# Optimization experiments

Measured on AMD Instinct MI355X. Metric: run time of the kernel, lower is better.

## Reference

```python
import jax, jax.numpy as jnp
import numpy as np

B, S, D, H = 2, 2048, 1024, 16
HD = D // H  # head_dim = 64
THETA = 10000.0


def setup_inputs() -> dict:
    key = jax.random.key(0)
    ks = jax.random.split(key, 7)
    sd = 1.0 / np.sqrt(D)
    return {
        "hidden_states": jax.random.normal(ks[0], (B, S, D), jnp.float32),
        "attention_mask": jnp.ones((B, S), jnp.int32),
        "Wq": jax.random.normal(ks[1], (D, D), jnp.float32) * sd,
        "Wk": jax.random.normal(ks[2], (D, D), jnp.float32) * sd,
        "Wv": jax.random.normal(ks[3], (D, D), jnp.float32) * sd,
        "Wo": jax.random.normal(ks[4], (D, D), jnp.float32) * sd,
        "bo": jnp.zeros((D,), jnp.float32),
        "rel_bias": jax.random.normal(ks[5], (H, S, S), jnp.float32) * 0.02,
    }


def _rope_tables(seq_len):
    inv_freq = 1.0 / (THETA ** (jnp.arange(0, HD, 2, dtype=jnp.float32) / HD))  # [HD/2]
    freqs = jnp.arange(seq_len, dtype=jnp.float32)[:, None] * inv_freq[None, :]  # [S, HD/2]
    # add a heads axis for broadcasting against [B, S, H, HD/2]
    return jnp.cos(freqs)[:, None, :], jnp.sin(freqs)[:, None, :]


def _apply_rope(x, cos, sin):
    # x: [B, S, H, HD]; interleaved even/odd rotation
    x1, x2 = x[..., 0::2], x[..., 1::2]
    r1 = x1 * cos - x2 * sin
    r2 = x1 * sin + x2 * cos
    return jnp.stack([r1, r2], axis=-1).reshape(x.shape)


def reference(hidden_states, attention_mask, Wq, Wk, Wv, Wo, bo, rel_bias):
    b, s, d = hidden_states.shape
    q = (hidden_states @ Wq.T).reshape(b, s, H, HD)
    k = (hidden_states @ Wk.T).reshape(b, s, H, HD)
    v = (hidden_states @ Wv.T).reshape(b, s, H, HD)

    cos, sin = _rope_tables(s)
    q = _apply_rope(q, cos, sin)
    k = _apply_rope(k, cos, sin)

    scale = HD ** -0.5
    scores = jnp.einsum('bqhd,bkhd->bhqk', q, k) * scale + rel_bias[None]
    scores = jnp.where(attention_mask[:, None, None, :] == 0, -jnp.inf, scores)
    attn = jax.nn.softmax(scores, axis=-1)  # dropout is identity in eval
    out = jnp.einsum('bhqk,bkhd->bqhd', attn, v).reshape(b, s, d)
    return out @ Wo.T + bo
```

## Files before the change

kernel.cpp:

```cpp
#include <hip/hip_runtime.h>

typedef unsigned short u16;
typedef short bf16x8 __attribute__((ext_vector_type(8)));
typedef float f32x4 __attribute__((ext_vector_type(4)));
typedef unsigned short u16x4 __attribute__((ext_vector_type(4)));

typedef const __attribute__((address_space(1))) unsigned int* gas_ptr;
typedef __attribute__((address_space(3))) unsigned int* las_ptr;

__device__ __forceinline__ void gl_lds16(const void* g, void* l) {
  __builtin_amdgcn_global_load_lds((gas_ptr)g, (las_ptr)l, 16, 0, 0);
}

__device__ __forceinline__ u16 f2bf(float f) {
  union { float f; unsigned u; } v; v.f = f;
  unsigned r = v.u + 0x7FFFu + ((v.u >> 16) & 1u);
  return (u16)(r >> 16);
}

__global__ void k_rope_tables(float* __restrict__ ctab, float* __restrict__ stab) {
  int t = blockIdx.x * 256 + threadIdx.x;
  int s = t >> 5, tt = t & 31;
  double f = exp(-((double)(2 * tt) / 64.0) * log(10000.0));
  double a = (double)s * f;
  ctab[t] = (float)cos(a);
  stab[t] = (float)sin(a);
}

__device__ __forceinline__ void store_bf4(u16* p, float4 v) {
  u16x4 o; o[0] = f2bf(v.x); o[1] = f2bf(v.y); o[2] = f2bf(v.z); o[3] = f2bf(v.w);
  *(u16x4*)p = o;
}

__global__ void k_convert(const float* __restrict__ hs, const float* __restrict__ Wq,
                          const float* __restrict__ Wk, const float* __restrict__ Wv,
                          const float* __restrict__ Wo,
                          u16* __restrict__ Xb, u16* __restrict__ Wqkv, u16* __restrict__ Wob) {
  int e = (blockIdx.x * 256 + threadIdx.x) * 4;
  const int R1 = 4096 * 1024, R2 = R1 + 3072 * 1024;
  if (e < R1) {
    store_bf4(Xb + e, *(const float4*)&hs[e]);
  } else if (e < R2) {
    int w = e - R1; int row = w >> 10, col = w & 1023;
    const float* src = row < 1024 ? &Wq[(size_t)row * 1024]
                     : (row < 2048 ? &Wk[(size_t)(row - 1024) * 1024]
                                   : &Wv[(size_t)(row - 2048) * 1024]);
    store_bf4(Wqkv + w, *(const float4*)&src[col]);
  } else {
    int w = e - R2;
    store_bf4(Wob + w, *(const float4*)&Wo[w]);
  }
}

__global__ __launch_bounds__(256, 3)
void k_gemm_bt(const u16* __restrict__ A, const u16* __restrict__ B,
               const float* __restrict__ bias, float* __restrict__ C,
               int K, int ldc) {
  __shared__ u16 ldsA[128 * 64];
  __shared__ u16 ldsB[128 * 64];
  const int tid = threadIdx.x;
  const int bn = blockIdx.x, bm = blockIdx.y;
  const int lane = tid & 63, wave = tid >> 6;
  const int wm = wave >> 1, wn = wave & 1;
  const int l16 = lane & 15, quad = lane >> 4;

  const int srow = lane >> 3;
  const int scol = ((lane & 7) ^ srow) * 8;
  const u16* agb = A + (size_t)(bm * 128 + wave * 8 + srow) * K + scol;
  const u16* bgb = B + (size_t)(bn * 128 + wave * 8 + srow) * K + scol;

  const f32x4 vzero = {0.f, 0.f, 0.f, 0.f};
  f32x4 acc[4][4];
#pragma unroll
  for (int i = 0; i < 4; ++i)
#pragma unroll
    for (int j = 0; j < 4; ++j) acc[i][j] = vzero;

  const int xq = l16 & 7;
  const int NKT = K >> 6;
  for (int kt = 0; kt < NKT; ++kt) {
    __syncthreads();
#pragma unroll
    for (int p = 0; p < 4; ++p) {
      gl_lds16(agb + (size_t)p * 32 * K + kt * 64, &ldsA[(p * 4 + wave) * 512]);
      gl_lds16(bgb + (size_t)p * 32 * K + kt * 64, &ldsB[(p * 4 + wave) * 512]);
    }
    __syncthreads();
#pragma unroll
    for (int ks = 0; ks < 2; ++ks) {
      bf16x8 af[4], bfr[4];
#pragma unroll
      for (int mi = 0; mi < 4; ++mi)
        af[mi] = *(const bf16x8*)&ldsA[(wm * 64 + mi * 16 + l16) * 64 + ((ks * 4 + quad) ^ xq) * 8];
#pragma unroll
      for (int ni = 0; ni < 4; ++ni)
        bfr[ni] = *(const bf16x8*)&ldsB[(wn * 64 + ni * 16 + l16) * 64 + ((ks * 4 + quad) ^ xq) * 8];
#pragma unroll
      for (int mi = 0; mi < 4; ++mi)
#pragma unroll
        for (int ni = 0; ni < 4; ++ni)
          acc[mi][ni] = __builtin_amdgcn_mfma_f32_16x16x32_bf16(af[mi], bfr[ni], acc[mi][ni], 0, 0, 0);
    }
  }

  const int row0 = bm * 128 + wm * 64, col0 = bn * 128 + wn * 64;
#pragma unroll
  for (int mi = 0; mi < 4; ++mi)
#pragma unroll
    for (int ni = 0; ni < 4; ++ni) {
      int col = col0 + ni * 16 + l16;
      float badd = bias ? bias[col] : 0.f;
#pragma unroll
      for (int rr = 0; rr < 4; ++rr) {
        int row = row0 + mi * 16 + quad * 4 + rr;
        C[(size_t)row * ldc + col] = acc[mi][ni][rr] + badd;
      }
    }
}

__global__ void k_rope_apply(const float* __restrict__ QKV, const float* __restrict__ ctab,
                             const float* __restrict__ stab,
                             u16* __restrict__ Qb, u16* __restrict__ Kb) {
  int t = blockIdx.x * 256 + threadIdx.x;
  int i = t >> 9;
  int c = t & 511; int h = c >> 5, tt = c & 31;
  int s = i & 2047, b = i >> 11;
  const float* base = QKV + (size_t)i * 3072;
  float cs = ctab[s * 32 + tt], sn = stab[s * 32 + tt];
  float2 q = *(const float2*)&base[h * 64 + 2 * tt];
  float2 k = *(const float2*)&base[1024 + h * 64 + 2 * tt];
  size_t ob = ((size_t)(b * 16 + h) * 2048 + s) * 64 + 2 * tt;
  union { u16 h2[2]; unsigned u; } oq, ok;
  oq.h2[0] = f2bf((q.x * cs - q.y * sn) * 0.125f);
  oq.h2[1] = f2bf((q.x * sn + q.y * cs) * 0.125f);
  ok.h2[0] = f2bf(k.x * cs - k.y * sn);
  ok.h2[1] = f2bf(k.x * sn + k.y * cs);
  *(unsigned*)&Qb[ob] = oq.u;
  *(unsigned*)&Kb[ob] = ok.u;
}

__global__ void k_vtrans(const float* __restrict__ QKV, u16* __restrict__ Vtb) {
  __shared__ u16 T[64 * 72];
  int st = blockIdx.x & 31, bh = blockIdx.x >> 5;
  int tid = threadIdx.x;
  int b = bh >> 4, h = bh & 15;
  {
    int rr = tid >> 2;
    int dg = (tid & 3) * 16;
    const float* src = QKV + (size_t)(b * 2048 + st * 64 + rr) * 3072 + 2048 + h * 64 + dg;
#pragma unroll
    for (int j = 0; j < 4; ++j) {
      float4 v = *(const float4*)&src[j * 4];
      T[(dg + j * 4 + 0) * 72 + rr] = f2bf(v.x);
      T[(dg + j * 4 + 1) * 72 + rr] = f2bf(v.y);
      T[(dg + j * 4 + 2) * 72 + rr] = f2bf(v.z);
      T[(dg + j * 4 + 3) * 72 + rr] = f2bf(v.w);
    }
  }
  __syncthreads();
  int d = tid >> 2, cg = (tid & 3) * 2;
  u16* vo = Vtb + ((size_t)bh * 64 + d) * 2048 + st * 64;
  *(float4*)&vo[cg * 8]       = *(const float4*)&T[d * 72 + cg * 8];
  *(float4*)&vo[(cg + 1) * 8] = *(const float4*)&T[d * 72 + (cg + 1) * 8];
}

__global__ __launch_bounds__(256, 4)
void k_attn(const u16* __restrict__ Qb, const u16* __restrict__ Kb, const u16* __restrict__ Vtb,
            const float* __restrict__ rel_bias, const int* __restrict__ mask,
            u16* __restrict__ Ob) {
  __shared__ u16 Ks[2][64 * 64];
  __shared__ u16 Vs[2][64 * 64];
  __shared__ u16 Ps[64 * 64];

  const int tid = threadIdx.x;
  const int gid = blockIdx.x;
  const int b = gid & 1, h = (gid >> 1) & 15, qt = gid >> 5;
  const int bh = b * 16 + h;
  const int lane = tid & 63, w = tid >> 6;
  const int l16 = lane & 15, quad = lane >> 4;
  const int xq = l16 & 7;

  bf16x8 qreg[2];
  {
    const u16* qg = Qb + ((size_t)bh * 2048 + qt * 64 + w * 16 + l16) * 64 + quad * 8;
    qreg[0] = *(const bf16x8*)&qg[0];
    qreg[1] = *(const bf16x8*)&qg[32];
  }

  const int srow = lane >> 3;
  const int scol = ((lane & 7) ^ srow) * 8;
  const u16* kgb = Kb + ((size_t)bh * 2048 + w * 8 + srow) * 64 + scol;
  const u16* vgb = Vtb + ((size_t)bh * 64 + w * 8 + srow) * 2048 + scol;

  const float* bp[4];
#pragma unroll
  for (int rr = 0; rr < 4; ++rr)
    bp[rr] = rel_bias + ((size_t)h * 2048 + qt * 64 + w * 16 + quad * 4 + rr) * 2048 + l16;
  const int* mbase = mask + b * 2048 + l16;

  const f32x4 vzero = {0.f, 0.f, 0.f, 0.f};
  f32x4 accO[4];
  float ls[4] = {0.f, 0.f, 0.f, 0.f};
#pragma unroll
  for (int ni = 0; ni < 4; ++ni) accO[ni] = vzero;

  float brc[4][4], brn[4][4];
  int mkc[4], mkn[4];
#pragma unroll
  for (int ni = 0; ni < 4; ++ni) {
    mkc[ni] = mbase[ni * 16];
#pragma unroll
    for (int rr = 0; rr < 4; ++rr) brc[ni][rr] = bp[rr][ni * 16];
  }
  gl_lds16(kgb,               &Ks[0][(0 * 4 + w) * 512]);
  gl_lds16(kgb + 2048,        &Ks[0][(1 * 4 + w) * 512]);
  gl_lds16(vgb,               &Vs[0][(0 * 4 + w) * 512]);
  gl_lds16(vgb + 32 * 2048,   &Vs[0][(1 * 4 + w) * 512]);

  for (int t = 0; t < 32; ++t) {
    const int cur = t & 1, nxt = cur ^ 1;
    const int kt0 = t * 64;
    __syncthreads();

    if (t + 1 < 32) {
      gl_lds16(kgb + (kt0 + 64) * 64,        &Ks[nxt][(0 * 4 + w) * 512]);
      gl_lds16(kgb + (kt0 + 64) * 64 + 2048, &Ks[nxt][(1 * 4 + w) * 512]);
      gl_lds16(vgb + kt0 + 64,               &Vs[nxt][(0 * 4 + w) * 512]);
      gl_lds16(vgb + kt0 + 64 + 32 * 2048,   &Vs[nxt][(1 * 4 + w) * 512]);
#pragma unroll
      for (int ni = 0; ni < 4; ++ni) {
        mkn[ni] = mbase[kt0 + 64 + ni * 16];
#pragma unroll
        for (int rr = 0; rr < 4; ++rr) brn[ni][rr] = bp[rr][kt0 + 64 + ni * 16];
      }
    }

    f32x4 sa[4];
#pragma unroll
    for (int ni = 0; ni < 4; ++ni) sa[ni] = vzero;
#pragma unroll
    for (int ks = 0; ks < 2; ++ks) {
#pragma unroll
      for (int ni = 0; ni < 4; ++ni) {
        bf16x8 kf = *(const bf16x8*)&Ks[cur][(ni * 16 + l16) * 64 + ((ks * 4 + quad) ^ xq) * 8];
        sa[ni] = __builtin_amdgcn_mfma_f32_16x16x32_bf16(qreg[ks], kf, sa[ni], 0, 0, 0);
      }
    }

#pragma unroll
    for (int ni = 0; ni < 4; ++ni) {
#pragma unroll
      for (int rr = 0; rr < 4; ++rr) {
        float p = mkc[ni] ? __expf(sa[ni][rr] + brc[ni][rr] - 24.f) : 0.f;
        int prow = w * 16 + quad * 4 + rr;
        Ps[prow * 64 + (((ni * 2 + (l16 >> 3)) ^ (prow & 7)) << 3) + (l16 & 7)] = f2bf(p);
        ls[rr] += p;
      }
    }

#pragma unroll
    for (int ks = 0; ks < 2; ++ks) {
      bf16x8 pf = *(const bf16x8*)&Ps[(w * 16 + l16) * 64 + ((ks * 4 + quad) ^ xq) * 8];
#pragma unroll
      for (int ni = 0; ni < 4; ++ni) {
        bf16x8 vf = *(const bf16x8*)&Vs[cur][(ni * 16 + l16) * 64 + ((ks * 4 + quad) ^ xq) * 8];
        accO[ni] = __builtin_amdgcn_mfma_f32_16x16x32_bf16(pf, vf, accO[ni], 0, 0, 0);
      }
    }

#pragma unroll
    for (int ni = 0; ni < 4; ++ni) {
      mkc[ni] = mkn[ni];
#pragma unroll
      for (int rr = 0; rr < 4; ++rr) brc[ni][rr] = brn[ni][rr];
    }
  }

#pragma unroll
  for (int rr = 0; rr < 4; ++rr) {
#pragma unroll
    for (int d = 1; d < 16; d <<= 1) ls[rr] += __shfl_xor(ls[rr], d, 16);
  }
#pragma unroll
  for (int rr = 0; rr < 4; ++rr) {
    float inv = 1.f / ls[rr];
    int row = qt * 64 + w * 16 + quad * 4 + rr;
#pragma unroll
    for (int ni = 0; ni < 4; ++ni)
      Ob[(((size_t)b * 2048 + row) * 16 + h) * 64 + ni * 16 + l16] = f2bf(accO[ni][rr] * inv);
  }
}

extern "C" void kernel_launch(void* const* d_in, const int* in_sizes, int n_in,
                              void* d_out, int out_size, void* d_ws, size_t ws_size,
                              hipStream_t stream) {
  (void)in_sizes; (void)n_in; (void)out_size; (void)ws_size;
  const float* hs  = (const float*)d_in[0];
  const int*   msk = (const int*)d_in[1];
  const float* Wq  = (const float*)d_in[2];
  const float* Wk  = (const float*)d_in[3];
  const float* Wv  = (const float*)d_in[4];
  const float* Wo  = (const float*)d_in[5];
  const float* bo  = (const float*)d_in[6];
  const float* rb  = (const float*)d_in[7];
  float* out = (float*)d_out;

  char* ws = (char*)d_ws;
  size_t off = 0;
  auto alloc = [&](size_t n) { char* p = ws + off; off += (n + 255) & ~(size_t)255; return p; };
  float* QKV  = (float*)alloc(4096UL * 3072 * 4);
  u16*   Xb   = (u16*)  alloc(4096UL * 1024 * 2);
  u16*   Wqkv = (u16*)  alloc(3072UL * 1024 * 2);
  u16*   Wob  = (u16*)  alloc(1024UL * 1024 * 2);
  u16*   Qb   = (u16*)  alloc(4096UL * 1024 * 2);
  u16*   Kb   = (u16*)  alloc(4096UL * 1024 * 2);
  u16*   Vtb  = (u16*)  alloc(4096UL * 1024 * 2);
  float* ctab = (float*)alloc(2048UL * 32 * 4);
  float* stab = (float*)alloc(2048UL * 32 * 4);
  u16*   Ob   = Xb;

  k_rope_tables<<<256, 256, 0, stream>>>(ctab, stab);
  k_convert<<<8192, 256, 0, stream>>>(hs, Wq, Wk, Wv, Wo, Xb, Wqkv, Wob);
  k_gemm_bt<<<dim3(24, 32), 256, 0, stream>>>(Xb, Wqkv, nullptr, QKV, 1024, 3072);
  k_rope_apply<<<8192, 256, 0, stream>>>(QKV, ctab, stab, Qb, Kb);
  k_vtrans<<<1024, 256, 0, stream>>>(QKV, Vtb);
  k_attn<<<1024, 256, 0, stream>>>(Qb, Kb, Vtb, rb, msk, Ob);
  k_gemm_bt<<<dim3(8, 32), 256, 0, stream>>>(Ob, Wob, bo, out, 1024, 1024);
}
```

Before: 523.6 us.

## Fuse RoPE and V transpose into QKV GEMM epilogue, fold tables into convert

Merges the RoPE table computation into the convert kernel. RoPE, the Q scale and the V transpose become part of the QKV GEMM epilogue, which writes bf16 Q/K/Vt directly. This removes the fp32 QKV intermediate and two extra kernel launches. The attention softmax switches to exp2 with the bias pre-scaled and the mask folded into the bias registers, and the block order now iterates heads fastest. The output projection uses a new 128x64-tile GEMM to double the block count. Risks include scattered strided stores for Vt in the epilogue and redundant table loads per element.

```diff
diff --git a/kernel.cpp b/kernel.cpp
--- a/kernel.cpp
+++ b/kernel.cpp
@@ -18,44 +18,47 @@
   return (u16)(r >> 16);
 }
 
-__global__ void k_rope_tables(float* __restrict__ ctab, float* __restrict__ stab) {
-  int t = blockIdx.x * 256 + threadIdx.x;
-  int s = t >> 5, tt = t & 31;
-  double f = exp(-((double)(2 * tt) / 64.0) * log(10000.0));
-  double a = (double)s * f;
-  ctab[t] = (float)cos(a);
-  stab[t] = (float)sin(a);
-}
-
-__device__ __forceinline__ void store_bf4(u16* p, float4 v) {
-  u16x4 o; o[0] = f2bf(v.x); o[1] = f2bf(v.y); o[2] = f2bf(v.z); o[3] = f2bf(v.w);
-  *(u16x4*)p = o;
+__device__ __forceinline__ float fexp2(float x) {
+  float r; asm("v_exp_f32 %0, %1" : "=v"(r) : "v"(x)); return r;
 }
 
 __global__ void k_convert(const float* __restrict__ hs, const float* __restrict__ Wq,
                           const float* __restrict__ Wk, const float* __restrict__ Wv,
                           const float* __restrict__ Wo,
-                          u16* __restrict__ Xb, u16* __restrict__ Wqkv, u16* __restrict__ Wob) {
+                          u16* __restrict__ Xb, u16* __restrict__ Wqkv, u16* __restrict__ Wob,
+                          float* __restrict__ ctab, float* __restrict__ stab) {
+  if (blockIdx.x >= 8192) {
+    int t = (blockIdx.x - 8192) * 256 + threadIdx.x;
+    int s = t >> 5, tt = t & 31;
+    double f = exp(-((double)(2 * tt) / 64.0) * log(10000.0));
+    double a = (double)s * f;
+    ctab[t] = (float)cos(a);
+    stab[t] = (float)sin(a);
+    return;
+  }
   int e = (blockIdx.x * 256 + threadIdx.x) * 4;
   const int R1 = 4096 * 1024, R2 = R1 + 3072 * 1024;
+  float4 v; u16* dst;
   if (e < R1) {
-    store_bf4(Xb + e, *(const float4*)&hs[e]);
+    v = *(const float4*)&hs[e]; dst = Xb + e;
   } else if (e < R2) {
     int w = e - R1; int row = w >> 10, col = w & 1023;
     const float* src = row < 1024 ? &Wq[(size_t)row * 1024]
                      : (row < 2048 ? &Wk[(size_t)(row - 1024) * 1024]
                                    : &Wv[(size_t)(row - 2048) * 1024]);
-    store_bf4(Wqkv + w, *(const float4*)&src[col]);
+    v = *(const float4*)&src[col]; dst = Wqkv + w;
   } else {
-    int w = e - R2;
-    store_bf4(Wob + w, *(const float4*)&Wo[w]);
-  }
+    int w = e - R2; v = *(const float4*)&Wo[w]; dst = Wob + w;
+  }
+  u16x4 o; o[0] = f2bf(v.x); o[1] = f2bf(v.y); o[2] = f2bf(v.z); o[3] = f2bf(v.w);
+  *(u16x4*)dst = o;
 }
 
 __global__ __launch_bounds__(256, 3)
-void k_gemm_bt(const u16* __restrict__ A, const u16* __restrict__ B,
-               const float* __restrict__ bias, float* __restrict__ C,
-               int K, int ldc) {
+void k_gemm_qkv(const u16* __restrict__ A, const u16* __restrict__ B,
+                const float* __restrict__ ctab, const float* __restrict__ stab,
+                u16* __restrict__ Qb, u16* __restrict__ Kb, u16* __restrict__ Vtb,
+                int K) {
   __shared__ u16 ldsA[128 * 64];
   __shared__ u16 ldsB[128 * 64];
   const int tid = threadIdx.x;
@@ -104,64 +107,52 @@
   }
 
   const int row0 = bm * 128 + wm * 64, col0 = bn * 128 + wn * 64;
-#pragma unroll
-  for (int mi = 0; mi < 4; ++mi)
-#pragma unroll
-    for (int ni = 0; ni < 4; ++ni) {
-      int col = col0 + ni * 16 + l16;
-      float badd = bias ? bias[col] : 0.f;
-#pragma unroll
-      for (int rr = 0; rr < 4; ++rr) {
-        int row = row0 + mi * 16 + quad * 4 + rr;
-        C[(size_t)row * ldc + col] = acc[mi][ni][rr] + badd;
-      }
-    }
-}
-
-__global__ void k_rope_apply(const float* __restrict__ QKV, const float* __restrict__ ctab,
-                             const float* __restrict__ stab,
-                             u16* __restrict__ Qb, u16* __restrict__ Kb) {
-  int t = blockIdx.x * 256 + threadIdx.x;
-  int i = t >> 9;
-  int c = t & 511; int h = c >> 5, tt = c & 31;
-  int s = i & 2047, b = i >> 11;
-  const float* base = QKV + (size_t)i * 3072;
-  float cs = ctab[s * 32 + tt], sn = stab[s * 32 + tt];
-  float2 q = *(const float2*)&base[h * 64 + 2 * tt];
-  float2 k = *(const float2*)&base[1024 + h * 64 + 2 * tt];
-  size_t ob = ((size_t)(b * 16 + h) * 2048 + s) * 64 + 2 * tt;
-  union { u16 h2[2]; unsigned u; } oq, ok;
-  oq.h2[0] = f2bf((q.x * cs - q.y * sn) * 0.125f);
-  oq.h2[1] = f2bf((q.x * sn + q.y * cs) * 0.125f);
-  ok.h2[0] = f2bf(k.x * cs - k.y * sn);
-  ok.h2[1] = f2bf(k.x * sn + k.y * cs);
-  *(unsigned*)&Qb[ob] = oq.u;
-  *(unsigned*)&Kb[ob] = ok.u;
-}
-
-__global__ void k_vtrans(const float* __restrict__ QKV, u16* __restrict__ Vtb) {
-  __shared__ u16 T[64 * 72];
-  int st = blockIdx.x & 31, bh = blockIdx.x >> 5;
-  int tid = threadIdx.x;
-  int b = bh >> 4, h = bh & 15;
-  {
-    int rr = tid >> 2;
-    int dg = (tid & 3) * 16;
-    const float* src = QKV + (size_t)(b * 2048 + st * 64 + rr) * 3072 + 2048 + h * 64 + dg;
-#pragma unroll
-    for (int j = 0; j < 4; ++j) {
-      float4 v = *(const float4*)&src[j * 4];
-      T[(dg + j * 4 + 0) * 72 + rr] = f2bf(v.x);
-      T[(dg + j * 4 + 1) * 72 + rr] = f2bf(v.y);
-      T[(dg + j * 4 + 2) * 72 + rr] = f2bf(v.z);
-      T[(dg + j * 4 + 3) * 72 + rr] = f2bf(v.w);
-    }
-  }
-  __syncthreads();
-  int d = tid >> 2, cg = (tid & 3) * 2;
-  u16* vo = Vtb + ((size_t)bh * 64 + d) * 2048 + st * 64;
-  *(float4*)&vo[cg * 8]       = *(const float4*)&T[d * 72 + cg * 8];
-  *(float4*)&vo[(cg + 1) * 8] = *(const float4*)&T[d * 72 + (cg + 1) * 8];
+  const int sect = bn >> 3;
+
+  if (sect < 2) {
+    u16* dst = sect == 0 ? Qb : Kb;
+    const float mul = sect == 0 ? 0.18033688f : 1.0f;
+#pragma unroll
+    for (int mi = 0; mi < 4; ++mi)
+#pragma unroll
+      for (int ni = 0; ni < 4; ++ni) {
+        int col = col0 + ni * 16 + l16;
+        int cc = col & 1023;
+        int h = cc >> 6, tt = (cc & 63) >> 1;
+#pragma unroll
+        for (int rr = 0; rr < 4; ++rr) {
+          int row = row0 + mi * 16 + quad * 4 + rr;
+          int s = row & 2047, bb = row >> 11;
+          float x = acc[mi][ni][rr];
+          float xo = __shfl_xor(x, 1);
+          float x1 = (l16 & 1) ? xo : x;
+          float x2 = (l16 & 1) ? x : xo;
+          float cs = ctab[s * 32 + tt], sn = stab[s * 32 + tt];
+          float r1 = (x1 * cs - x2 * sn) * mul;
+          float r2 = (x1 * sn + x2 * cs) * mul;
+          if (!(l16 & 1)) {
+            union { u16 h2[2]; unsigned u; } o;
+            o.h2[0] = f2bf(r1); o.h2[1] = f2bf(r2);
+            *(unsigned*)&dst[((size_t)(bb * 16 + h) * 2048 + s) * 64 + (cc & 63)] = o.u;
+          }
+        }
+      }
+  } else {
+#pragma unroll
+    for (int mi = 0; mi < 4; ++mi)
+#pragma unroll
+      for (int ni = 0; ni < 4; ++ni) {
+        int col = col0 + ni * 16 + l16;
+        int cc = col & 1023;
+        int h = cc >> 6, d = cc & 63;
+        int row = row0 + mi * 16 + quad * 4;
+        int s = row & 2047, bb = row >> 11;
+        u16x4 o;
+        o[0] = f2bf(acc[mi][ni][0]); o[1] = f2bf(acc[mi][ni][1]);
+        o[2] = f2bf(acc[mi][ni][2]); o[3] = f2bf(acc[mi][ni][3]);
+        *(u16x4*)&Vtb[((size_t)(bb * 16 + h) * 64 + d) * 2048 + s] = o;
+      }
+  }
 }
 
 __global__ __launch_bounds__(256, 4)
@@ -174,7 +165,7 @@
 
   const int tid = threadIdx.x;
   const int gid = blockIdx.x;
-  const int b = gid & 1, h = (gid >> 1) & 15, qt = gid >> 5;
+  const int h = gid & 15, b = (gid >> 4) & 1, qt = gid >> 5;
   const int bh = b * 16 + h;
   const int lane = tid & 63, w = tid >> 6;
   const int l16 = lane & 15, quad = lane >> 4;
@@ -205,12 +196,14 @@
   for (int ni = 0; ni < 4; ++ni) accO[ni] = vzero;
 
   float brc[4][4], brn[4][4];
-  int mkc[4], mkn[4];
 #pragma unroll
   for (int ni = 0; ni < 4; ++ni) {
-    mkc[ni] = mbase[ni * 16];
-#pragma unroll
-    for (int rr = 0; rr < 4; ++rr) brc[ni][rr] = bp[rr][ni * 16];
+    int mk = mbase[ni * 16];
+#pragma unroll
+    for (int rr = 0; rr < 4; ++rr) {
+      float bv = bp[rr][ni * 16];
+      brc[ni][rr] = mk ? bv * 1.44269504f - 34.6246810f : -1e30f;
+    }
   }
   gl_lds16(kgb,               &Ks[0][(0 * 4 + w) * 512]);
   gl_lds16(kgb + 2048,        &Ks[0][(1 * 4 + w) * 512]);
@@ -229,9 +222,12 @@
       gl_lds16(vgb + kt0 + 64 + 32 * 2048,   &Vs[nxt][(1 * 4 + w) * 512]);
 #pragma unroll
       for (int ni = 0; ni < 4; ++ni) {
-        mkn[ni] = mbase[kt0 + 64 + ni * 16];
-#pragma unroll
-        for (int rr = 0; rr < 4; ++rr) brn[ni][rr] = bp[rr][kt0 + 64 + ni * 16];
+        int mk = mbase[kt0 + 64 + ni * 16];
+#pragma unroll
+        for (int rr = 0; rr < 4; ++rr) {
+          float bv = bp[rr][kt0 + 64 + ni * 16];
+          brn[ni][rr] = mk ? bv * 1.44269504f - 34.6246810f : -1e30f;
+        }
       }
     }
 
@@ -251,7 +247,7 @@
     for (int ni = 0; ni < 4; ++ni) {
 #pragma unroll
       for (int rr = 0; rr < 4; ++rr) {
-        float p = mkc[ni] ? __expf(sa[ni][rr] + brc[ni][rr] - 24.f) : 0.f;
+        float p = fexp2(sa[ni][rr] + brc[ni][rr]);
         int prow = w * 16 + quad * 4 + rr;
         Ps[prow * 64 + (((ni * 2 + (l16 >> 3)) ^ (prow & 7)) << 3) + (l16 & 7)] = f2bf(p);
         ls[rr] += p;
@@ -269,11 +265,9 @@
     }
 
 #pragma unroll
-    for (int ni = 0; ni < 4; ++ni) {
-      mkc[ni] = mkn[ni];
+    for (int ni = 0; ni < 4; ++ni)
 #pragma unroll
       for (int rr = 0; rr < 4; ++rr) brc[ni][rr] = brn[ni][rr];
-    }
   }
 
 #pragma unroll
@@ -289,6 +283,73 @@
     for (int ni = 0; ni < 4; ++ni)
       Ob[(((size_t)b * 2048 + row) * 16 + h) * 64 + ni * 16 + l16] = f2bf(accO[ni][rr] * inv);
   }
+}
+
+__global__ __launch_bounds__(256, 2)
+void k_gemm_n64(const u16* __restrict__ A, const u16* __restrict__ B,
+                const float* __restrict__ bias, float* __restrict__ C,
+                int K, int ldc) {
+  __shared__ u16 ldsA[128 * 64];
+  __shared__ u16 ldsB[64 * 64];
+  const int tid = threadIdx.x;
+  const int bn = blockIdx.x, bm = blockIdx.y;
+  const int lane = tid & 63, wave = tid >> 6;
+  const int wm = wave >> 1, wn = wave & 1;
+  const int l16 = lane & 15, quad = lane >> 4;
+
+  const int srow = lane >> 3;
+  const int scol = ((lane & 7) ^ srow) * 8;
+  const u16* agb = A + (size_t)(bm * 128 + wave * 8 + srow) * K + scol;
+  const u16* bgb = B + (size_t)(bn * 64 + wave * 8 + srow) * K + scol;
+
+  const f32x4 vzero = {0.f, 0.f, 0.f, 0.f};
+  f32x4 acc[4][2];
+#pragma unroll
+  for (int i = 0; i < 4; ++i)
+#pragma unroll
+    for (int j = 0; j < 2; ++j) acc[i][j] = vzero;
+
+  const int xq = l16 & 7;
+  const int NKT = K >> 6;
+  for (int kt = 0; kt < NKT; ++kt) {
+    __syncthreads();
+#pragma unroll
+    for (int p = 0; p < 4; ++p)
+      gl_lds16(agb + (size_t)p * 32 * K + kt * 64, &ldsA[(p * 4 + wave) * 512]);
+#pragma unroll
+    for (int p = 0; p < 2; ++p)
+      gl_lds16(bgb + (size_t)p * 32 * K + kt * 64, &ldsB[(p * 4 + wave) * 512]);
+    __syncthreads();
+#pragma unroll
+    for (int ks = 0; ks < 2; ++ks) {
+      bf16x8 af[4], bfr[2];
+#pragma unroll
+      for (int mi = 0; mi < 4; ++mi)
+        af[mi] = *(const bf16x8*)&ldsA[(wm * 64 + mi * 16 + l16) * 64 + ((ks * 4 + quad) ^ xq) * 8];
+#pragma unroll
+      for (int ni = 0; ni < 2; ++ni)
+        bfr[ni] = *(const bf16x8*)&ldsB[(wn * 32 + ni * 16 + l16) * 64 + ((ks * 4 + quad) ^ xq) * 8];
+#pragma unroll
+      for (int mi = 0; mi < 4; ++mi)
+#pragma unroll
+        for (int ni = 0; ni < 2; ++ni)
+          acc[mi][ni] = __builtin_amdgcn_mfma_f32_16x16x32_bf16(af[mi], bfr[ni], acc[mi][ni], 0, 0, 0);
+    }
+  }
+
+  const int row0 = bm * 128 + wm * 64, col0 = bn * 64 + wn * 32;
+#pragma unroll
+  for (int mi = 0; mi < 4; ++mi)
+#pragma unroll
+    for (int ni = 0; ni < 2; ++ni) {
+      int col = col0 + ni * 16 + l16;
+      float badd = bias ? bias[col] : 0.f;
+#pragma unroll
+      for (int rr = 0; rr < 4; ++rr) {
+        int row = row0 + mi * 16 + quad * 4 + rr;
+        C[(size_t)row * ldc + col] = acc[mi][ni][rr] + badd;
+      }
+    }
 }
 
 extern "C" void kernel_launch(void* const* d_in, const int* in_sizes, int n_in,
@@ -308,7 +369,6 @@
   char* ws = (char*)d_ws;
   size_t off = 0;
   auto alloc = [&](size_t n) { char* p = ws + off; off += (n + 255) & ~(size_t)255; return p; };
-  float* QKV  = (float*)alloc(4096UL * 3072 * 4);
   u16*   Xb   = (u16*)  alloc(4096UL * 1024 * 2);
   u16*   Wqkv = (u16*)  alloc(3072UL * 1024 * 2);
   u16*   Wob  = (u16*)  alloc(1024UL * 1024 * 2);
@@ -319,11 +379,8 @@
   float* stab = (float*)alloc(2048UL * 32 * 4);
   u16*   Ob   = Xb;
 
-  k_rope_tables<<<256, 256, 0, stream>>>(ctab, stab);
-  k_convert<<<8192, 256, 0, stream>>>(hs, Wq, Wk, Wv, Wo, Xb, Wqkv, Wob);
-  k_gemm_bt<<<dim3(24, 32), 256, 0, stream>>>(Xb, Wqkv, nullptr, QKV, 1024, 3072);
-  k_rope_apply<<<8192, 256, 0, stream>>>(QKV, ctab, stab, Qb, Kb);
-  k_vtrans<<<1024, 256, 0, stream>>>(QKV, Vtb);
+  k_convert<<<8448, 256, 0, stream>>>(hs, Wq, Wk, Wv, Wo, Xb, Wqkv, Wob, ctab, stab);
+  k_gemm_qkv<<<dim3(24, 32), 256, 0, stream>>>(Xb, Wqkv, ctab, stab, Qb, Kb, Vtb, 1024);
   k_attn<<<1024, 256, 0, stream>>>(Qb, Kb, Vtb, rb, msk, Ob);
-  k_gemm_bt<<<dim3(8, 32), 256, 0, stream>>>(Ob, Wob, bo, out, 1024, 1024);
-}
+  k_gemm_n64<<<dim3(16, 32), 256, 0, stream>>>(Ob, Wob, bo, out, 1024, 1024);
+}
```

Result: faster. 508.5 us (-2.9%).
